# Performance work log

Measured on AMD Instinct MI355X. Metric: run time of the kernel, lower is better.

The kernel has to match this reference:

```python
import jax, jax.numpy as jnp
import numpy as np

N_AGENTS = 2
B, C, H, W = 4, 64, 200, 352


def _conv(x, w, b):
    # x: (n, Cin, H, W), w: (Cout, Cin, 3, 3), 'SAME' padding, stride 1
    y = jax.lax.conv_general_dilated(
        x, w, window_strides=(1, 1), padding='SAME',
        dimension_numbers=('NCHW', 'OIHW', 'NCHW'))
    return y + b[None, :, None, None]


def setup_inputs() -> dict:
    key = jax.random.key(0)
    ks = jax.random.split(key, 4)
    s = 0.05  # small init so sigmoid/tanh stay in useful range
    x = jax.random.normal(ks[0], (N_AGENTS, B, C, H, W), dtype=jnp.float32)
    msg_w = jax.random.normal(ks[1], (C, 2 * C, 3, 3), dtype=jnp.float32) * s
    msg_b = jnp.zeros((C,), jnp.float32)
    gates_w = jax.random.normal(ks[2], (2 * C, 3 * C, 3, 3), dtype=jnp.float32) * s
    gates_b = jnp.zeros((2 * C,), jnp.float32)
    can_w = jax.random.normal(ks[3], (C, 3 * C, 3, 3), dtype=jnp.float32) * s
    can_b = jnp.zeros((C,), jnp.float32)
    return {'x': x, 'msg_w': msg_w, 'msg_b': msg_b,
            'gates_w': gates_w, 'gates_b': gates_b,
            'can_w': can_w, 'can_b': can_b}


def reference(x, msg_w, msg_b, gates_w, gates_b, can_w, can_b):
    # num_iteration=1; only new_x[0] (agent 0's updated feature) is returned,
    # so we compute exactly that path.
    x0, x1 = x[0], x[1]                       # each (B, C, H, W)
    neighbor = jnp.concatenate([x0, x1], axis=1)   # (B, 2C, H, W)
    message = _conv(neighbor, msg_w, msg_b)        # (B, C, H, W)
    agg = 0.5 * (x0 + message)                     # 'avg' over stacked pair
    cat_feat = jnp.concatenate([x0, agg], axis=1)  # (B, 2C, H, W)

    # ConvGRU: batch_first input (1, B, 2C, H, W) -> sequence length B, batch 1
    h0 = jnp.zeros((1, C, H, W), cat_feat.dtype)

    def step(h, inp):
        inp = inp[None]                                     # (1, 2C, H, W)
        comb = jnp.concatenate([inp, h], axis=1)            # (1, 3C, H, W)
        gates = jax.nn.sigmoid(_conv(comb, gates_w, gates_b))
        reset, update = jnp.split(gates, 2, axis=1)         # each (1, C, H, W)
        comb2 = jnp.concatenate([inp, reset * h], axis=1)
        cnm = jnp.tanh(_conv(comb2, can_w, can_b))
        h_next = (1.0 - update) * h + update * cnm
        return h_next, h_next[0]

    _, out = jax.lax.scan(step, h0, cat_feat)  # out: (B, C, H, W)
    return out
```

## Files before the change

### kernel.cpp

```cpp
#include <hip/hip_runtime.h>
#include <math.h>
#include <string.h>

#define HH 200
#define WW 352
#define HWSZ (HH*WW)
#define CHW (64L*HWSZ)

enum { EPI_MSG=0, EPI_GATES=1, EPI_CAND=2 };

typedef __attribute__((ext_vector_type(8))) _Float16 f16x8;
typedef __attribute__((ext_vector_type(4))) float f32x4;
typedef __attribute__((ext_vector_type(4))) unsigned int uint4v;
typedef __attribute__((ext_vector_type(4))) unsigned short ushort4v;

__device__ __forceinline__ unsigned short f2h(float f) {
    _Float16 h = (_Float16)f;
    return __builtin_bit_cast(unsigned short, h);
}
__device__ __forceinline__ float h2f(unsigned short u) {
    return (float)__builtin_bit_cast(_Float16, u);
}

__device__ __forceinline__ void load_lds16(const unsigned short* g,
                                           unsigned short* l) {
    __builtin_amdgcn_global_load_lds(
        (const __attribute__((address_space(1))) unsigned int*)g,
        (__attribute__((address_space(3))) unsigned int*)l, 16, 0, 0);
}

__global__ void prepack_k(const float* __restrict__ mw,
                          const float* __restrict__ gw,
                          const float* __restrict__ cw,
                          unsigned short* __restrict__ pw,
                          unsigned short* __restrict__ zp)
{
    const int MSG_I = 4*18432;
    const int GAT_I = 12*18432;
    const int CAN_I = 6*18432;
    const int TOTAL = MSG_I + GAT_I + CAN_I;
    int idx = blockIdx.x*256 + threadIdx.x;
    if (idx >= TOTAL) {
        int r = idx - TOTAL;
        if (r < 128) zp[r] = 0;
        return;
    }
    const float* w; int cin, nkb, rel; unsigned short* base;
    if (idx < MSG_I)              { w=mw; cin=128; nkb=4; rel=idx;              base=pw; }
    else if (idx < MSG_I+GAT_I)   { w=gw; cin=192; nkb=6; rel=idx-MSG_I;        base=pw+73728; }
    else                          { w=cw; cin=192; nkb=6; rel=idx-MSG_I-GAT_I;  base=pw+294912; }
    int chunk = rel / 18432, r = rel - chunk*18432;
    int j = r & 7, lane = (r >> 3) & 63, cfsh = r >> 9;
    int cf = cfsh & 3, sh = cfsh >> 2;
    int q = lane >> 4, n16 = lane & 15;
    int co_l = cf*16 + n16, ch = q*8 + j;
    int cogrp = chunk / nkb, kb = chunk - cogrp*nkb;
    float f = w[(((long)(cogrp*64 + co_l))*cin + kb*32 + ch)*9 + sh];
    base[(size_t)chunk*18432 + r] = f2h(f);
}

__global__ void convert_all_k(const float* __restrict__ x,
                              unsigned short* __restrict__ xb0_all,
                              unsigned short* __restrict__ xb1_all)
{
    int idx = blockIdx.x*256 + threadIdx.x;
    int cp   = idx & 15;
    int rest = idx >> 4;
    int px4  = rest % 17600;
    int r2   = rest / 17600;
    int hb = r2 & 1, ag = (r2 >> 1) & 1, t = r2 >> 2;
    const float* src = x + ((size_t)(ag*4 + t))*CHW
                         + (size_t)(hb*32 + 2*cp)*HWSZ + (size_t)px4*4;
    float4 a = *(const float4*)src;
    float4 b = *(const float4*)(src + HWSZ);
    unsigned int* dst = (unsigned int*)((ag ? xb1_all : xb0_all)
                        + (size_t)t*CHW + (size_t)hb*HWSZ*32) + (size_t)px4*64 + cp;
    dst[0]  = (unsigned)f2h(a.x) | ((unsigned)f2h(b.x) << 16);
    dst[16] = (unsigned)f2h(a.y) | ((unsigned)f2h(b.y) << 16);
    dst[32] = (unsigned)f2h(a.z) | ((unsigned)f2h(b.z) << 16);
    dst[48] = (unsigned)f2h(a.w) | ((unsigned)f2h(b.w) << 16);
}

template<int EPI, int WR>
__global__ __launch_bounds__(256, 2)
void conv_mfma_k(const unsigned short* __restrict__ seg0b,
                 const unsigned short* __restrict__ seg1b,
                 const unsigned short* __restrict__ seg2b,
                 int nkb, int nkb_stride, int grp_base,
                 const unsigned short* __restrict__ pw,
                 const unsigned short* __restrict__ zp,
                 const float* __restrict__ bias,
                 const unsigned short* e_hb,
                 const unsigned short* __restrict__ e_updb,
                 float* out_f,
                 unsigned short* out_b,
                 unsigned short* out_b2)
{
    constexpr int ROWS   = 4*WR;
    constexpr int PP     = 2*WR;
    constexpr int POS    = (ROWS+2)*34;
    constexpr int HSLOTS = (68 + 2*ROWS)*4;
    constexpr int HEXT   = HSLOTS - 256;

    __shared__ unsigned short s_in0[POS*32];
    __shared__ unsigned short s_in1[POS*32];
    __shared__ unsigned short s_w[9*4*64*8];

    const int tid  = threadIdx.x;
    const int lane = tid & 63;
    const int wv   = tid >> 6;
    const int n16  = lane & 15;
    const int q    = lane >> 4;

    int grp, ts = 0;
    if (EPI == EPI_MSG) { ts = blockIdx.z; grp = 0; }
    else                { grp = blockIdx.z + grp_base; }

    const unsigned short* s0 = seg0b + (EPI==EPI_MSG ? (size_t)ts*CHW : 0);
    const unsigned short* s1 = seg1b + (EPI==EPI_MSG ? (size_t)ts*CHW : 0);
    unsigned short* ob = out_b;
    if (EPI == EPI_MSG) ob = (ts < 3) ? out_b + (size_t)ts*CHW : out_b2;

    const int x0p = blockIdx.x * 32;
    const int y0  = blockIdx.y * ROWS;

    int hdst0 = 0, hdst1 = 0; size_t hsrc0 = 0, hsrc1 = 0;
    bool hval0 = false, hval1 = false;
    {
        auto hcalc = [&](int s, int& hdst, size_t& hsrc, bool& hval) {
            int hp = s >> 2, gs = s & 3;
            int row, col;
            if (hp < 34)      { row = 0;      col = hp; }
            else if (hp < 68) { row = ROWS+1; col = hp - 34; }
            else { int k = hp - 68; row = 1 + (k >> 1); col = (k & 1) * 33; }
            int pos = row*34 + col;
            int gy = y0 + row - 1, gx = x0p + col - 1;
            hdst = (pos << 5) + (gs << 3);
            int g = (gs ^ pos ^ (pos >> 2)) & 3;
            if ((unsigned)gy < (unsigned)HH && (unsigned)gx < (unsigned)WW) {
                hval = true;
                hsrc = ((size_t)(gy*WW + gx) << 5) + (size_t)(g << 3);
            }
        };
        hcalc(tid, hdst0, hsrc0, hval0);
        if (tid < HEXT) hcalc(tid + 256, hdst1, hsrc1, hval1);
    }

    auto srcof = [&](int kb) -> const unsigned short* {
        return ((kb < 2) ? s0 : (kb < 4) ? s1 : seg2b) + (size_t)(kb & 1)*HWSZ*32;
    };

    struct HV { uint4v a, b; };
    auto halo_load = [&](int kb, HV& h) {
        const unsigned short* src = srcof(kb);
        h.a = *(const uint4v*)(hval0 ? src + hsrc0 : zp);
        if (tid < HEXT) h.b = *(const uint4v*)(hval1 ? src + hsrc1 : zp);
    };
    auto halo_write = [&](unsigned short* bin, const HV& h) {
        *(uint4v*)&bin[hdst0] = h.a;
        if (tid < HEXT) *(uint4v*)&bin[hdst1] = h.b;
    };

    auto stage_in = [&](int kb, unsigned short* bin) {
        const unsigned short* src = srcof(kb);
#pragma unroll
        for (int j = 0; j < 2*WR; ++j) {
            const int c    = wv + 4*j;
            const int row  = 1 + (c >> 1);
            const int colh = c & 1;
            const int gy   = y0 + row - 1;
            const int p0   = row*34 + 1 + colh*16;
            const int pl   = p0 + (lane >> 2);
            const int g    = ((lane & 3) ^ pl ^ (pl >> 2)) & 3;
            const int gx   = x0p + colh*16 + (lane >> 2);
            load_lds16(src + (((size_t)(gy*WW + gx)) << 5) + (g << 3),
                       &bin[(size_t)p0 << 5]);
        }
    };
    auto stage_w = [&](int kb) {
        const unsigned short* wsrc = pw + (size_t)(grp*nkb_stride + kb)*18432;
#pragma unroll
        for (int i = 0; i < 9; ++i) {
            const int u = wv + 4*i;
            load_lds16(wsrc + (size_t)u*512 + (size_t)lane*8, &s_w[(size_t)u*512]);
        }
    };

    f32x4 acc[4][PP];
#pragma unroll
    for (int cf=0; cf<4; ++cf)
#pragma unroll
        for (int p=0; p<PP; ++p) acc[cf][p] = (f32x4){0.f,0.f,0.f,0.f};

    auto compute = [&](const unsigned short* sin) {
#pragma unroll
        for (int ky = 0; ky < 3; ++ky) {
#pragma unroll
            for (int kx = 0; kx < 3; ++kx) {
                const int sh = ky*3 + kx;
                f16x8 aw[4];
#pragma unroll
                for (int cf = 0; cf < 4; ++cf)
                    aw[cf] = *(const f16x8*)&s_w[((sh*4 + cf)*64 + lane)*8];
#pragma unroll
                for (int p = 0; p < PP; ++p) {
                    const int rl = (WR == 2 ? 2*wv + (p >> 1) : wv) + ky;
                    const int cl = 16*(WR == 2 ? (p & 1) : p) + n16 + kx;
                    const int pos = rl*34 + cl;
                    const int sw = (q ^ pos ^ (pos >> 2)) & 3;
                    f16x8 bfr = *(const f16x8*)&sin[(pos << 5) + (sw << 3)];
#pragma unroll
                    for (int cf = 0; cf < 4; ++cf)
                        acc[cf][p] = __builtin_amdgcn_mfma_f32_16x16x32_f16(
                                         aw[cf], bfr, acc[cf][p], 0, 0, 0);
                }
            }
        }
    };

    HV h0, h1;
    stage_in(0, s_in0);
    stage_w(0);
    halo_load(0, h0);

    for (int kb = 0; kb < nkb; kb += 2) {
        halo_write(s_in0, h0);
        __syncthreads();
        halo_load(kb + 1, h1);
        stage_in(kb + 1, s_in1);
        __builtin_amdgcn_sched_barrier(0);
        compute(s_in0);
        __syncthreads();
        stage_w(kb + 1);
        halo_write(s_in1, h1);
        __syncthreads();
        if (kb + 2 < nkb) {
            halo_load(kb + 2, h0);
            stage_in(kb + 2, s_in0);
            __builtin_amdgcn_sched_barrier(0);
        }
        compute(s_in1);
        __syncthreads();
        if (kb + 2 < nkb) stage_w(kb + 2);
    }

#pragma unroll
    for (int cf = 0; cf < 4; ++cf) {
        const int half   = cf >> 1;
        const int cobase = grp*64 + cf*16 + q*4;
        const int cmod   = (cf & 1)*16 + q*4;
#pragma unroll
        for (int p = 0; p < PP; ++p) {
            const int row = y0 + (WR == 2 ? 2*wv + (p >> 1) : wv);
            const int col = x0p + 16*(WR == 2 ? (p & 1) : p) + n16;
            if (row >= HH) continue;
            const long pix = (long)row*WW + col;
            const size_t iidx = (((size_t)half*HWSZ + pix) << 5) + cmod;
            float v[4];
#pragma unroll
            for (int r = 0; r < 4; ++r) v[r] = acc[cf][p][r] + bias[cobase + r];

            if (EPI == EPI_MSG) {
                ushort4v xv = *(const ushort4v*)&s0[iidx];
                ushort4v s;
#pragma unroll
                for (int r = 0; r < 4; ++r)
                    s[r] = f2h(0.5f*(h2f(xv[r]) + v[r]));
                *(ushort4v*)&ob[iidx] = s;
            } else if (EPI == EPI_GATES) {
                if (grp == 0) {
                    ushort4v hv = e_hb ? *(const ushort4v*)&e_hb[iidx]
                                       : (ushort4v){0,0,0,0};
                    ushort4v s;
#pragma unroll
                    for (int r = 0; r < 4; ++r) {
                        float g = 1.f/(1.f + __expf(-v[r]));
                        s[r] = f2h(g * h2f(hv[r]));
                    }
                    *(ushort4v*)&out_b[iidx] = s;
                } else {
                    ushort4v s;
#pragma unroll
                    for (int r = 0; r < 4; ++r)
                        s[r] = f2h(1.f/(1.f + __expf(-v[r])));
                    *(ushort4v*)&out_b2[iidx] = s;
                }
            } else {
                ushort4v uv = *(const ushort4v*)&e_updb[iidx];
                ushort4v hv = e_hb ? *(const ushort4v*)&e_hb[iidx]
                                   : (ushort4v){0,0,0,0};
                ushort4v s;
#pragma unroll
                for (int r = 0; r < 4; ++r) {
                    float cnm = tanhf(v[r]);
                    float u   = h2f(uv[r]);
                    float hn  = (1.f - u)*h2f(hv[r]) + u*cnm;
                    out_f[(long)(cobase+r)*HWSZ + pix] = hn;
                    s[r] = f2h(hn);
                }
                *(ushort4v*)&out_b[iidx] = s;
            }
        }
    }
}

extern "C" void kernel_launch(void* const* d_in, const int* in_sizes, int n_in,
                              void* d_out, int out_size, void* d_ws, size_t ws_size,
                              hipStream_t stream)
{
    const float* x       = (const float*)d_in[0];
    const float* msg_w   = (const float*)d_in[1];
    const float* msg_b   = (const float*)d_in[2];
    const float* gates_w = (const float*)d_in[3];
    const float* gates_b = (const float*)d_in[4];
    const float* can_w   = (const float*)d_in[5];
    const float* can_b   = (const float*)d_in[6];
    float* out = (float*)d_out;

    unsigned short* W       = (unsigned short*)d_ws;
    unsigned short* xb0_all = W;
    unsigned short* aggb3   = W + 4*CHW;
    unsigned short* rhb     = W + 5*CHW;
    unsigned short* updb    = W + 6*CHW;
    unsigned short* hb      = W + 7*CHW;
    unsigned short* pw      = W + 8*CHW;
    unsigned short* pw_msg  = pw;
    unsigned short* pw_gat  = pw + 73728;
    unsigned short* pw_can  = pw + 294912;
    unsigned short* zp      = pw + 405504;

    unsigned short* outU16   = (unsigned short*)d_out;
    unsigned short* xb1_all  = outU16;
    unsigned short* aggbase  = outU16 + 4*CHW;

    prepack_k<<<dim3(1585), dim3(256), 0, stream>>>(msg_w, gates_w, can_w, pw, zp);
    convert_all_k<<<dim3(17600), dim3(256), 0, stream>>>(x, xb0_all, xb1_all);

    conv_mfma_k<EPI_MSG,2><<<dim3(11,25,4), dim3(256), 0, stream>>>(
        xb0_all, xb1_all, nullptr, 4, 4, 0, pw_msg, zp, msg_b,
        nullptr, nullptr, nullptr, aggbase, aggb3);

    for (int t = 0; t < 4; ++t) {
        const unsigned short* xt  = xb0_all + (size_t)t*CHW;
        const unsigned short* agt = (t < 3) ? aggbase + (size_t)t*CHW : aggb3;
        const unsigned short* hprev = t ? hb : nullptr;

        if (t == 0) {
            conv_mfma_k<EPI_GATES,1><<<dim3(11,50,1), dim3(256), 0, stream>>>(
                xt, agt, nullptr, 4, 6, 1, pw_gat, zp, gates_b,
                nullptr, nullptr, nullptr, rhb, updb);
        } else {
            conv_mfma_k<EPI_GATES,2><<<dim3(11,25,2), dim3(256), 0, stream>>>(
                xt, agt, hb, 6, 6, 0, pw_gat, zp, gates_b,
                hprev, nullptr, nullptr, rhb, updb);
        }
        conv_mfma_k<EPI_CAND,1><<<dim3(11,50,1), dim3(256), 0, stream>>>(
            xt, agt, rhb, t ? 6 : 4, 6, 0, pw_can, zp, can_b,
            hprev, updb, out + (size_t)t*CHW, hb, nullptr);
    }
}
```

Baseline: 406.8 us.

## Use 512-thread blocks with one output row per wave for all conv kernels

Replaces the WR template (256 threads, 4 or 8 rows per block) with a single 512-thread configuration. Each of 8 waves computes one output row of 32 pixels, so every block covers 8 rows. Staging, halo and weight loads are redistributed across 8 waves, and the row-bound check is dropped since 200 divides evenly by 8. The aim is more waves per CU and better latency hiding from fewer accumulators per thread, at the cost of less weight reuse per wave and a larger block synchronized at each barrier.

```diff
diff --git a/kernel.cpp b/kernel.cpp
--- a/kernel.cpp
+++ b/kernel.cpp
@@ -81,8 +81,8 @@
     dst[48] = (unsigned)f2h(a.w) | ((unsigned)f2h(b.w) << 16);
 }
 
-template<int EPI, int WR>
-__global__ __launch_bounds__(256, 2)
+template<int EPI>
+__global__ __launch_bounds__(512, 4)
 void conv_mfma_k(const unsigned short* __restrict__ seg0b,
                  const unsigned short* __restrict__ seg1b,
                  const unsigned short* __restrict__ seg2b,
@@ -96,14 +96,11 @@
                  unsigned short* out_b,
                  unsigned short* out_b2)
 {
-    constexpr int ROWS   = 4*WR;
-    constexpr int PP     = 2*WR;
-    constexpr int POS    = (ROWS+2)*34;
+    constexpr int ROWS   = 8;
     constexpr int HSLOTS = (68 + 2*ROWS)*4;
-    constexpr int HEXT   = HSLOTS - 256;
-
-    __shared__ unsigned short s_in0[POS*32];
-    __shared__ unsigned short s_in1[POS*32];
+
+    __shared__ unsigned short s_in0[(ROWS+2)*34*32];
+    __shared__ unsigned short s_in1[(ROWS+2)*34*32];
     __shared__ unsigned short s_w[9*4*64*8];
 
     const int tid  = threadIdx.x;
@@ -124,48 +121,41 @@
     const int x0p = blockIdx.x * 32;
     const int y0  = blockIdx.y * ROWS;
 
-    int hdst0 = 0, hdst1 = 0; size_t hsrc0 = 0, hsrc1 = 0;
-    bool hval0 = false, hval1 = false;
-    {
-        auto hcalc = [&](int s, int& hdst, size_t& hsrc, bool& hval) {
-            int hp = s >> 2, gs = s & 3;
-            int row, col;
-            if (hp < 34)      { row = 0;      col = hp; }
-            else if (hp < 68) { row = ROWS+1; col = hp - 34; }
-            else { int k = hp - 68; row = 1 + (k >> 1); col = (k & 1) * 33; }
-            int pos = row*34 + col;
-            int gy = y0 + row - 1, gx = x0p + col - 1;
-            hdst = (pos << 5) + (gs << 3);
-            int g = (gs ^ pos ^ (pos >> 2)) & 3;
-            if ((unsigned)gy < (unsigned)HH && (unsigned)gx < (unsigned)WW) {
-                hval = true;
-                hsrc = ((size_t)(gy*WW + gx) << 5) + (size_t)(g << 3);
-            }
-        };
-        hcalc(tid, hdst0, hsrc0, hval0);
-        if (tid < HEXT) hcalc(tid + 256, hdst1, hsrc1, hval1);
+    int hdst = 0; size_t hsrc = 0; bool hval = false;
+    const bool hact = (tid < HSLOTS);
+    if (hact) {
+        int hp = tid >> 2, gs = tid & 3;
+        int row, col;
+        if (hp < 34)      { row = 0;      col = hp; }
+        else if (hp < 68) { row = ROWS+1; col = hp - 34; }
+        else { int k = hp - 68; row = 1 + (k >> 1); col = (k & 1) * 33; }
+        int pos = row*34 + col;
+        int gy = y0 + row - 1, gx = x0p + col - 1;
+        hdst = (pos << 5) + (gs << 3);
+        int g = (gs ^ pos ^ (pos >> 2)) & 3;
+        if ((unsigned)gy < (unsigned)HH && (unsigned)gx < (unsigned)WW) {
+            hval = true;
+            hsrc = ((size_t)(gy*WW + gx) << 5) + (size_t)(g << 3);
+        }
     }
 
     auto srcof = [&](int kb) -> const unsigned short* {
         return ((kb < 2) ? s0 : (kb < 4) ? s1 : seg2b) + (size_t)(kb & 1)*HWSZ*32;
     };
 
-    struct HV { uint4v a, b; };
-    auto halo_load = [&](int kb, HV& h) {
+    auto halo_load = [&](int kb, uint4v& h) {
         const unsigned short* src = srcof(kb);
-        h.a = *(const uint4v*)(hval0 ? src + hsrc0 : zp);
-        if (tid < HEXT) h.b = *(const uint4v*)(hval1 ? src + hsrc1 : zp);
-    };
-    auto halo_write = [&](unsigned short* bin, const HV& h) {
-        *(uint4v*)&bin[hdst0] = h.a;
-        if (tid < HEXT) *(uint4v*)&bin[hdst1] = h.b;
+        if (hact) h = *(const uint4v*)(hval ? src + hsrc : zp);
+    };
+    auto halo_write = [&](unsigned short* bin, const uint4v& h) {
+        if (hact) *(uint4v*)&bin[hdst] = h;
     };
 
     auto stage_in = [&](int kb, unsigned short* bin) {
         const unsigned short* src = srcof(kb);
 #pragma unroll
-        for (int j = 0; j < 2*WR; ++j) {
-            const int c    = wv + 4*j;
+        for (int j = 0; j < 2; ++j) {
+            const int c    = wv + 8*j;
             const int row  = 1 + (c >> 1);
             const int colh = c & 1;
             const int gy   = y0 + row - 1;
@@ -180,17 +170,18 @@
     auto stage_w = [&](int kb) {
         const unsigned short* wsrc = pw + (size_t)(grp*nkb_stride + kb)*18432;
 #pragma unroll
-        for (int i = 0; i < 9; ++i) {
-            const int u = wv + 4*i;
-            load_lds16(wsrc + (size_t)u*512 + (size_t)lane*8, &s_w[(size_t)u*512]);
-        }
-    };
-
-    f32x4 acc[4][PP];
+        for (int i = 0; i < 5; ++i) {
+            const int u = wv + 8*i;
+            if (u < 36)
+                load_lds16(wsrc + (size_t)u*512 + (size_t)lane*8, &s_w[(size_t)u*512]);
+        }
+    };
+
+    f32x4 acc[4][2];
 #pragma unroll
     for (int cf=0; cf<4; ++cf)
 #pragma unroll
-        for (int p=0; p<PP; ++p) acc[cf][p] = (f32x4){0.f,0.f,0.f,0.f};
+        for (int p=0; p<2; ++p) acc[cf][p] = (f32x4){0.f,0.f,0.f,0.f};
 
     auto compute = [&](const unsigned short* sin) {
 #pragma unroll
@@ -203,9 +194,9 @@
                 for (int cf = 0; cf < 4; ++cf)
                     aw[cf] = *(const f16x8*)&s_w[((sh*4 + cf)*64 + lane)*8];
 #pragma unroll
-                for (int p = 0; p < PP; ++p) {
-                    const int rl = (WR == 2 ? 2*wv + (p >> 1) : wv) + ky;
-                    const int cl = 16*(WR == 2 ? (p & 1) : p) + n16 + kx;
+                for (int p = 0; p < 2; ++p) {
+                    const int rl = wv + ky;
+                    const int cl = 16*p + n16 + kx;
                     const int pos = rl*34 + cl;
                     const int sw = (q ^ pos ^ (pos >> 2)) & 3;
                     f16x8 bfr = *(const f16x8*)&sin[(pos << 5) + (sw << 3)];
@@ -218,7 +209,7 @@
         }
     };
 
-    HV h0, h1;
+    uint4v h0, h1;
     stage_in(0, s_in0);
     stage_w(0);
     halo_load(0, h0);
@@ -250,10 +241,9 @@
         const int cobase = grp*64 + cf*16 + q*4;
         const int cmod   = (cf & 1)*16 + q*4;
 #pragma unroll
-        for (int p = 0; p < PP; ++p) {
-            const int row = y0 + (WR == 2 ? 2*wv + (p >> 1) : wv);
-            const int col = x0p + 16*(WR == 2 ? (p & 1) : p) + n16;
-            if (row >= HH) continue;
+        for (int p = 0; p < 2; ++p) {
+            const int row = y0 + wv;
+            const int col = x0p + 16*p + n16;
             const long pix = (long)row*WW + col;
             const size_t iidx = (((size_t)half*HWSZ + pix) << 5) + cmod;
             float v[4];
@@ -336,7 +326,7 @@
     prepack_k<<<dim3(1585), dim3(256), 0, stream>>>(msg_w, gates_w, can_w, pw, zp);
     convert_all_k<<<dim3(17600), dim3(256), 0, stream>>>(x, xb0_all, xb1_all);
 
-    conv_mfma_k<EPI_MSG,2><<<dim3(11,25,4), dim3(256), 0, stream>>>(
+    conv_mfma_k<EPI_MSG><<<dim3(11,25,4), dim3(512), 0, stream>>>(
         xb0_all, xb1_all, nullptr, 4, 4, 0, pw_msg, zp, msg_b,
         nullptr, nullptr, nullptr, aggbase, aggb3);
 
@@ -346,15 +336,15 @@
         const unsigned short* hprev = t ? hb : nullptr;
 
         if (t == 0) {
-            conv_mfma_k<EPI_GATES,1><<<dim3(11,50,1), dim3(256), 0, stream>>>(
+            conv_mfma_k<EPI_GATES><<<dim3(11,25,1), dim3(512), 0, stream>>>(
                 xt, agt, nullptr, 4, 6, 1, pw_gat, zp, gates_b,
                 nullptr, nullptr, nullptr, rhb, updb);
         } else {
-            conv_mfma_k<EPI_GATES,2><<<dim3(11,25,2), dim3(256), 0, stream>>>(
+            conv_mfma_k<EPI_GATES><<<dim3(11,25,2), dim3(512), 0, stream>>>(
                 xt, agt, hb, 6, 6, 0, pw_gat, zp, gates_b,
                 hprev, nullptr, nullptr, rhb, updb);
         }
-        conv_mfma_k<EPI_CAND,1><<<dim3(11,50,1), dim3(256), 0, stream>>>(
+        conv_mfma_k<EPI_CAND><<<dim3(11,25,1), dim3(512), 0, stream>>>(
             xt, agt, rhb, t ? 6 : 4, 6, 0, pw_can, zp, can_b,
             hprev, updb, out + (size_t)t*CHW, hb, nullptr);
     }
```

Result: faster. 373.9 us (-8.1%).
